# Performance work log

Measured on AMD Instinct MI355X. Metric: run time of the kernel, lower is better.

## Reference

```python
import jax, jax.numpy as jnp
import numpy as np
import math

MODEL_DIM = 512
NUM_HEADS = 8
FFN_DIM = 2048
LN_EPS = 1e-5


def setup_inputs() -> dict:
    key = jax.random.key(0)
    ks = jax.random.split(key, 16)
    B, S, D, F = 1, 4096, MODEL_DIM, FFN_DIM
    s = 1.0 / math.sqrt(D)
    inp = {
        "x": jax.random.normal(ks[0], (B, S, D), dtype=jnp.float32),
        # Linear weights stored [in, out] (transpose of torch's [out, in]); y = x @ W + b
        "wq": jax.random.normal(ks[1], (D, D), dtype=jnp.float32) * s,
        "bq": jnp.zeros((D,), dtype=jnp.float32),
        "wk": jax.random.normal(ks[2], (D, D), dtype=jnp.float32) * s,
        "bk": jnp.zeros((D,), dtype=jnp.float32),
        "wv": jax.random.normal(ks[3], (D, D), dtype=jnp.float32) * s,
        "bv": jnp.zeros((D,), dtype=jnp.float32),
        "wo": jax.random.normal(ks[4], (D, D), dtype=jnp.float32) * s,
        "bo": jnp.zeros((D,), dtype=jnp.float32),
        "w1": jax.random.normal(ks[5], (D, F), dtype=jnp.float32) * s,
        "b1": jnp.zeros((F,), dtype=jnp.float32),
        "w2": jax.random.normal(ks[6], (F, D), dtype=jnp.float32) * (1.0 / math.sqrt(F)),
        "b2": jnp.zeros((D,), dtype=jnp.float32),
        "gamma": jnp.ones((D,), dtype=jnp.float32),
        "beta": jnp.zeros((D,), dtype=jnp.float32),
    }
    return inp


def _layer_norm(x, gamma, beta):
    mu = jnp.mean(x, axis=-1, keepdims=True)
    var = jnp.mean(jnp.square(x - mu), axis=-1, keepdims=True)
    return (x - mu) * jax.lax.rsqrt(var + LN_EPS) * gamma + beta


def reference(x, wq, bq, wk, bk, wv, bv, wo, bo, w1, b1, w2, b2, gamma, beta):
    B, S, D = x.shape
    H = NUM_HEADS
    dph = D // H
    q = x @ wq + bq
    k = x @ wk + bk
    v = x @ wv + bv
    # Faithful to original: direct view [B,S,D] -> [B*H, S, dph] (no head transpose)
    q = q.reshape(B * H, S, dph)
    k = k.reshape(B * H, S, dph)
    v = v.reshape(B * H, S, dph)
    scores = jnp.einsum('bqd,bkd->bqk', q, k) / math.sqrt(dph)  # [B*H, S, S]
    attn = jax.nn.softmax(scores, axis=-1)
    context = jnp.einsum('bqk,bkd->bqd', attn, v).reshape(B, S, D)
    attn_out = context @ wo + bo + x  # residual (dropout is identity in eval)
    ffn = jax.nn.relu(attn_out @ w1 + b1) @ w2 + b2
    out = _layer_norm(ffn + attn_out, gamma, beta)
    return out, attn
```

## Files before the change

### kernel.cpp

```cpp
#include <hip/hip_runtime.h>
#include <hip/hip_bf16.h>
#include <cstdint>
#include <cstddef>

#define SEQ 4096
#define DM  512
#define NH  8
#define DPH 64
#define FF  2048

using short8 = __attribute__((ext_vector_type(8))) short;
using f32x4  = __attribute__((ext_vector_type(4))) float;

__device__ inline float b2f(unsigned short u) {
    union { unsigned int i; float f; } c; c.i = ((unsigned int)u) << 16; return c.f;
}
__device__ inline unsigned short f2b(float f) {
    union { float f; unsigned int u; } c; c.f = f;
    unsigned int u = c.u;
    return (unsigned short)((u + 0x7fffu + ((u >> 16) & 1u)) >> 16);
}

template<int BN, int NI>
__global__ __launch_bounds__(256) void tgemm_kernel(
    const unsigned short* __restrict__ A, const unsigned short* __restrict__ BT,
    const float* __restrict__ bias, const unsigned short* __restrict__ res,
    unsigned short* __restrict__ Cb, float* __restrict__ Cf,
    int M, int N, int K, int relu)
{
    __shared__ __align__(16) unsigned short As[128 * 40];
    __shared__ __align__(16) unsigned short Bs[BN * 40];

    const int t    = threadIdx.x;
    const int lane = t & 63;
    const int wid  = t >> 6;
    const int wr   = wid >> 1, wc = wid & 1;
    const int quad = lane >> 4, cl = lane & 15;
    const int m0 = blockIdx.y * 128;
    const int n0 = blockIdx.x * BN;

    const int srow = t >> 2;
    const int skc  = t & 3;

    const unsigned short* Arow0 = A  + (size_t)(m0 + srow) * K + skc * 8;
    const unsigned short* Arow1 = Arow0 + (size_t)64 * K;
    const unsigned short* Brow0 = BT + (size_t)(n0 + srow) * K + skc * 8;
    const unsigned short* Brow1 = Brow0 + (size_t)64 * K;

    f32x4 acc[4][NI];
    const f32x4 zero4 = {0.f, 0.f, 0.f, 0.f};
#pragma unroll
    for (int mi = 0; mi < 4; ++mi)
#pragma unroll
        for (int ni = 0; ni < NI; ++ni) acc[mi][ni] = zero4;

    short8 ar0, ar1, br0, br1;
    ar0 = *(const short8*)(Arow0);
    ar1 = *(const short8*)(Arow1);
    br0 = *(const short8*)(Brow0);
    if constexpr (NI == 4) br1 = *(const short8*)(Brow1);

    for (int k0 = 0; k0 < K; k0 += 32) {
        __syncthreads();
        *(short8*)(&As[srow * 40 + skc * 8])        = ar0;
        *(short8*)(&As[(srow + 64) * 40 + skc * 8]) = ar1;
        *(short8*)(&Bs[srow * 40 + skc * 8])        = br0;
        if constexpr (NI == 4) *(short8*)(&Bs[(srow + 64) * 40 + skc * 8]) = br1;
        __syncthreads();

        const int kn = k0 + 32;
        if (kn < K) {
            ar0 = *(const short8*)(Arow0 + kn);
            ar1 = *(const short8*)(Arow1 + kn);
            br0 = *(const short8*)(Brow0 + kn);
            if constexpr (NI == 4) br1 = *(const short8*)(Brow1 + kn);
        }

        short8 af[4], bf[NI];
#pragma unroll
        for (int mi = 0; mi < 4; ++mi)
            af[mi] = *(const short8*)(&As[(wr * 64 + mi * 16 + cl) * 40 + quad * 8]);
#pragma unroll
        for (int ni = 0; ni < NI; ++ni)
            bf[ni] = *(const short8*)(&Bs[(wc * (BN / 2) + ni * 16 + cl) * 40 + quad * 8]);
#pragma unroll
        for (int mi = 0; mi < 4; ++mi)
#pragma unroll
            for (int ni = 0; ni < NI; ++ni)
                acc[mi][ni] = __builtin_amdgcn_mfma_f32_16x16x32_bf16(af[mi], bf[ni], acc[mi][ni], 0, 0, 0);
    }

#pragma unroll
    for (int ni = 0; ni < NI; ++ni) {
        const int n = n0 + wc * (BN / 2) + ni * 16 + cl;
        const float bv = bias ? bias[n] : 0.f;
#pragma unroll
        for (int mi = 0; mi < 4; ++mi) {
#pragma unroll
            for (int r = 0; r < 4; ++r) {
                const int row = m0 + wr * 64 + mi * 16 + quad * 4 + r;
                float v = acc[mi][ni][r] + bv;
                const size_t idx = (size_t)row * N + n;
                if (res)  v += b2f(res[idx]);
                if (relu) v = fmaxf(v, 0.f);
                if (Cf) Cf[idx] = v;
                else    Cb[idx] = f2b(v);
            }
        }
    }
}

__global__ __launch_bounds__(256) void transpose_cast_kernel(
    const float* __restrict__ src, unsigned short* __restrict__ dst, int R, int C)
{
    __shared__ float tile[32][33];
    const int c0 = blockIdx.x * 32, r0 = blockIdx.y * 32;
    const int tx = threadIdx.x & 31, ty = threadIdx.x >> 5;
#pragma unroll
    for (int i = 0; i < 4; ++i)
        tile[ty + i * 8][tx] = src[(size_t)(r0 + ty + i * 8) * C + c0 + tx];
    __syncthreads();
#pragma unroll
    for (int i = 0; i < 4; ++i)
        dst[(size_t)(c0 + ty + i * 8) * R + r0 + tx] = f2b(tile[tx][ty + i * 8]);
}

__global__ __launch_bounds__(256) void transpose_kernel(
    const unsigned short* __restrict__ src, unsigned short* __restrict__ dst,
    int R, int C)
{
    __shared__ unsigned short tile[32][33];
    const long off = (long)blockIdx.z * (long)R * (long)C;
    src += off; dst += off;
    const int c0 = blockIdx.x * 32, r0 = blockIdx.y * 32;
    const int tx = threadIdx.x & 31, ty = threadIdx.x >> 5;
#pragma unroll
    for (int i = 0; i < 4; ++i)
        tile[ty + i * 8][tx] = src[(size_t)(r0 + ty + i * 8) * C + c0 + tx];
    __syncthreads();
#pragma unroll
    for (int i = 0; i < 4; ++i)
        dst[(size_t)(c0 + ty + i * 8) * R + r0 + tx] = tile[tx][ty + i * 8];
}

__global__ __launch_bounds__(256) void cast_kernel(
    const float* __restrict__ src, unsigned short* __restrict__ dst, int n4)
{
    const int i = blockIdx.x * 256 + threadIdx.x;
    if (i >= n4) return;
    const float4 v = ((const float4*)src)[i];
    union { unsigned short s[4]; unsigned long long u; } p;
    p.s[0] = f2b(v.x); p.s[1] = f2b(v.y); p.s[2] = f2b(v.z); p.s[3] = f2b(v.w);
    ((unsigned long long*)dst)[i] = p.u;
}

__global__ __launch_bounds__(256, 8) void fused_attn_kernel(
    const unsigned short* __restrict__ qb,
    const unsigned short* __restrict__ kb,
    const unsigned short* __restrict__ vT,
    float* __restrict__ att,
    unsigned short* __restrict__ ctx)
{
    __shared__ __align__(16) float Pl[4][16 * 36];
    __shared__ float smM[4][16];
    __shared__ float smS[4][16];
    __shared__ __align__(16) float cbuf[2][16 * 68];

    const int id    = blockIdx.x;
    const int h     = id & 7;
    const int strip = id >> 3;
    const int lane  = threadIdx.x & 63;
    const int w     = threadIdx.x >> 6;
    const int quad  = lane >> 4, col = lane & 15;
    const int m0    = strip * 16;

    const unsigned short* Qh = qb + (size_t)h * SEQ * DPH;
    const unsigned short* Kh = kb + (size_t)h * SEQ * DPH;
    const unsigned short* Vh = vT + (size_t)h * SEQ * DPH;
    float* atth = att + (size_t)h * SEQ * SEQ;
    unsigned short* ctxh = ctx + (size_t)h * SEQ * DPH;

    const unsigned short* qrow = Qh + (size_t)(m0 + col) * DPH + quad * 8;
    const short8 aq0 = *(const short8*)(qrow);
    const short8 aq1 = *(const short8*)(qrow + 32);

    const unsigned short* kbase = Kh + (size_t)(w * 1024 + col) * DPH + quad * 8;
    const float SC = 0.125f;
    const f32x4 zero4 = {0.f, 0.f, 0.f, 0.f};

    float m[4], s[4];
#pragma unroll
    for (int r = 0; r < 4; ++r) { m[r] = -1e30f; s[r] = 0.f; }

#pragma unroll 2
    for (int nt = 0; nt < 64; ++nt) {
        const unsigned short* kr = kbase + (size_t)nt * 16 * DPH;
        const short8 b0 = *(const short8*)(kr);
        const short8 b1 = *(const short8*)(kr + 32);
        f32x4 acc = zero4;
        acc = __builtin_amdgcn_mfma_f32_16x16x32_bf16(aq0, b0, acc, 0, 0, 0);
        acc = __builtin_amdgcn_mfma_f32_16x16x32_bf16(aq1, b1, acc, 0, 0, 0);
#pragma unroll
        for (int r = 0; r < 4; ++r) {
            const float v  = acc[r] * SC;
            const float nm = fmaxf(m[r], v);
            const float e  = __expf(fminf(m[r], v) - nm);
            s[r] = (v > m[r]) ? fmaf(s[r], e, 1.f) : (s[r] + e);
            m[r] = nm;
        }
    }
#pragma unroll
    for (int off = 1; off < 16; off <<= 1) {
#pragma unroll
        for (int r = 0; r < 4; ++r) {
            const float mo = __shfl_xor(m[r], off);
            const float so = __shfl_xor(s[r], off);
            const float nm = fmaxf(m[r], mo);
            s[r] = s[r] * __expf(m[r] - nm) + so * __expf(mo - nm);
            m[r] = nm;
        }
    }
    if (col == 0) {
#pragma unroll
        for (int r = 0; r < 4; ++r) { smM[w][quad * 4 + r] = m[r]; smS[w][quad * 4 + r] = s[r]; }
    }
    __syncthreads();
    float inv[4];
#pragma unroll
    for (int r = 0; r < 4; ++r) {
        const int row = quad * 4 + r;
        float M = smM[0][row], S = smS[0][row];
#pragma unroll
        for (int ww = 1; ww < 4; ++ww) {
            const float mo = smM[ww][row];
            const float so = smS[ww][row];
            const float nm = fmaxf(M, mo);
            S = S * __expf(M - nm) + so * __expf(mo - nm);
            M = nm;
        }
        m[r] = M;
        inv[r] = 1.f / S;
    }

    f32x4 cacc[4];
#pragma unroll
    for (int t = 0; t < 4; ++t) cacc[t] = zero4;

    float* Pw = Pl[w];
    float* abase = atth + (size_t)m0 * SEQ + w * 1024;
    const int srow2  = lane >> 3;
    const int schunk = lane & 7;
    for (int pr = 0; pr < 32; ++pr) {
#pragma unroll
        for (int sub = 0; sub < 2; ++sub) {
            const int ntl = pr * 2 + sub;
            const unsigned short* kr = kbase + (size_t)ntl * 16 * DPH;
            const short8 b0 = *(const short8*)(kr);
            const short8 b1 = *(const short8*)(kr + 32);
            f32x4 acc = zero4;
            acc = __builtin_amdgcn_mfma_f32_16x16x32_bf16(aq0, b0, acc, 0, 0, 0);
            acc = __builtin_amdgcn_mfma_f32_16x16x32_bf16(aq1, b1, acc, 0, 0, 0);
#pragma unroll
            for (int r = 0; r < 4; ++r) {
                const float p = __expf(fmaf(acc[r], SC, -m[r])) * inv[r];
                Pw[(quad * 4 + r) * 36 + sub * 16 + col] = p;
            }
        }
#pragma unroll
        for (int sset = 0; sset < 2; ++sset) {
            const int prow = srow2 + sset * 8;
            const float4 pv = *(const float4*)(Pw + prow * 36 + schunk * 4);
            *(float4*)(abase + (size_t)prow * SEQ + pr * 32 + schunk * 4) = pv;
        }
        const float4 pa0 = *(const float4*)(Pw + col * 36 + quad * 8);
        const float4 pa1 = *(const float4*)(Pw + col * 36 + quad * 8 + 4);
        union { unsigned short us[8]; short8 v; } ap;
        ap.us[0] = f2b(pa0.x); ap.us[1] = f2b(pa0.y);
        ap.us[2] = f2b(pa0.z); ap.us[3] = f2b(pa0.w);
        ap.us[4] = f2b(pa1.x); ap.us[5] = f2b(pa1.y);
        ap.us[6] = f2b(pa1.z); ap.us[7] = f2b(pa1.w);

        const int kg = w * 1024 + pr * 32;
        const unsigned short* vb0 = Vh + (size_t)col * SEQ + kg + quad * 8;
#pragma unroll
        for (int t = 0; t < 4; ++t) {
            const short8 bv = *(const short8*)(vb0 + (size_t)t * 16 * SEQ);
            cacc[t] = __builtin_amdgcn_mfma_f32_16x16x32_bf16(ap.v, bv, cacc[t], 0, 0, 0);
        }
    }

    if (w & 1) {
        float* cb = cbuf[w >> 1];
#pragma unroll
        for (int t = 0; t < 4; ++t)
#pragma unroll
            for (int r = 0; r < 4; ++r)
                cb[(quad * 4 + r) * 68 + t * 16 + col] = cacc[t][r];
    }
    __syncthreads();
    if (!(w & 1)) {
        const float* cb = cbuf[w >> 1];
#pragma unroll
        for (int t = 0; t < 4; ++t)
#pragma unroll
            for (int r = 0; r < 4; ++r)
                cacc[t][r] += cb[(quad * 4 + r) * 68 + t * 16 + col];
    }
    __syncthreads();
    if (w == 2) {
#pragma unroll
        for (int t = 0; t < 4; ++t)
#pragma unroll
            for (int r = 0; r < 4; ++r)
                cbuf[0][(quad * 4 + r) * 68 + t * 16 + col] = cacc[t][r];
    }
    __syncthreads();
    if (w == 0) {
#pragma unroll
        for (int t = 0; t < 4; ++t) {
#pragma unroll
            for (int r = 0; r < 4; ++r) {
                const float v = cacc[t][r] + cbuf[0][(quad * 4 + r) * 68 + t * 16 + col];
                ctxh[(size_t)(m0 + quad * 4 + r) * DPH + t * 16 + col] = f2b(v);
            }
        }
    }
}

__global__ __launch_bounds__(256) void ln_kernel(
    const float* __restrict__ pre,
    const float* __restrict__ gamma, const float* __restrict__ beta,
    float* __restrict__ out)
{
    __shared__ float redS[4], redQ[4];
    const float* p = pre + (size_t)blockIdx.x * 512;
    const int t = threadIdx.x;
    const int w = t >> 6, lane = t & 63;

    const float2 xv = *(const float2*)(p + t * 2);
    float s = xv.x + xv.y;
    float q = xv.x * xv.x + xv.y * xv.y;
#pragma unroll
    for (int off = 32; off; off >>= 1) {
        s += __shfl_xor(s, off);
        q += __shfl_xor(q, off);
    }
    if (lane == 0) { redS[w] = s; redQ[w] = q; }
    __syncthreads();
    s = redS[0] + redS[1] + redS[2] + redS[3];
    q = redQ[0] + redQ[1] + redQ[2] + redQ[3];

    const float mu  = s * (1.f / 512.f);
    const float var = q * (1.f / 512.f) - mu * mu;
    const float rs  = rsqrtf(var + 1e-5f);

    const size_t o = (size_t)blockIdx.x * 512 + t * 2;
    out[o]     = (xv.x - mu) * rs * gamma[t * 2]     + beta[t * 2];
    out[o + 1] = (xv.y - mu) * rs * gamma[t * 2 + 1] + beta[t * 2 + 1];
}

extern "C" void kernel_launch(void* const* d_in, const int* in_sizes, int n_in,
                              void* d_out, int out_size, void* d_ws, size_t ws_size,
                              hipStream_t stream)
{
    (void)in_sizes; (void)n_in; (void)out_size; (void)ws_size;

    const float* x     = (const float*)d_in[0];
    const float* wq    = (const float*)d_in[1];
    const float* bq    = (const float*)d_in[2];
    const float* wk    = (const float*)d_in[3];
    const float* bk    = (const float*)d_in[4];
    const float* wv    = (const float*)d_in[5];
    const float* bv    = (const float*)d_in[6];
    const float* wo    = (const float*)d_in[7];
    const float* bo    = (const float*)d_in[8];
    const float* w1    = (const float*)d_in[9];
    const float* b1    = (const float*)d_in[10];
    const float* w2    = (const float*)d_in[11];
    const float* b2    = (const float*)d_in[12];
    const float* gamma = (const float*)d_in[13];
    const float* beta  = (const float*)d_in[14];

    float* out = (float*)d_out;
    float* att = out + (size_t)SEQ * DM;

    char* wsp = (char*)d_ws;
    auto alloc = [&](size_t bytes) {
        char* p = wsp;
        wsp += (bytes + 255) & ~(size_t)255;
        return p;
    };
    unsigned short* wqT  = (unsigned short*)alloc((size_t)DM * DM * 2);
    unsigned short* wkT  = (unsigned short*)alloc((size_t)DM * DM * 2);
    unsigned short* wvT  = (unsigned short*)alloc((size_t)DM * DM * 2);
    unsigned short* woT  = (unsigned short*)alloc((size_t)DM * DM * 2);
    unsigned short* w1T  = (unsigned short*)alloc((size_t)DM * FF * 2);
    unsigned short* w2T  = (unsigned short*)alloc((size_t)FF * DM * 2);
    unsigned short* xb   = (unsigned short*)alloc((size_t)SEQ * DM * 2);
    unsigned short* qb   = (unsigned short*)alloc((size_t)SEQ * DM * 2);
    unsigned short* kb   = (unsigned short*)alloc((size_t)SEQ * DM * 2);
    unsigned short* vb   = (unsigned short*)alloc((size_t)SEQ * DM * 2);
    unsigned short* vT   = (unsigned short*)alloc((size_t)SEQ * DM * 2);
    unsigned short* ctx  = (unsigned short*)alloc((size_t)SEQ * DM * 2);
    unsigned short* aout = (unsigned short*)alloc((size_t)SEQ * DM * 2);
    unsigned short* ffn1 = (unsigned short*)alloc((size_t)SEQ * FF * 2);
    float*          pre  = (float*)alloc((size_t)SEQ * DM * 4);

    const dim3 blk(256);

    cast_kernel<<<dim3((SEQ * DM / 4 + 255) / 256), blk, 0, stream>>>(x, xb, SEQ * DM / 4);

    transpose_cast_kernel<<<dim3(16, 16), blk, 0, stream>>>(wq, wqT, DM, DM);
    transpose_cast_kernel<<<dim3(16, 16), blk, 0, stream>>>(wk, wkT, DM, DM);
    transpose_cast_kernel<<<dim3(16, 16), blk, 0, stream>>>(wv, wvT, DM, DM);
    transpose_cast_kernel<<<dim3(16, 16), blk, 0, stream>>>(wo, woT, DM, DM);
    transpose_cast_kernel<<<dim3(64, 16), blk, 0, stream>>>(w1, w1T, DM, FF);
    transpose_cast_kernel<<<dim3(16, 64), blk, 0, stream>>>(w2, w2T, FF, DM);

    tgemm_kernel<64, 2><<<dim3(8, 32), blk, 0, stream>>>(xb, wqT, bq, nullptr, qb, nullptr,
                                                         SEQ, DM, DM, 0);
    tgemm_kernel<64, 2><<<dim3(8, 32), blk, 0, stream>>>(xb, wkT, bk, nullptr, kb, nullptr,
                                                         SEQ, DM, DM, 0);
    tgemm_kernel<64, 2><<<dim3(8, 32), blk, 0, stream>>>(xb, wvT, bv, nullptr, vb, nullptr,
                                                         SEQ, DM, DM, 0);

    transpose_kernel<<<dim3(2, 128, 8), blk, 0, stream>>>(vb, vT, SEQ, DPH);

    fused_attn_kernel<<<dim3(2048), blk, 0, stream>>>(qb, kb, vT, att, ctx);

    tgemm_kernel<64, 2><<<dim3(8, 32), blk, 0, stream>>>(ctx, woT, bo, xb, aout, nullptr,
                                                         SEQ, DM, DM, 0);

    tgemm_kernel<128, 4><<<dim3(16, 32), blk, 0, stream>>>(aout, w1T, b1, nullptr, ffn1, nullptr,
                                                           SEQ, FF, DM, 1);

    tgemm_kernel<64, 2><<<dim3(8, 32), blk, 0, stream>>>(ffn1, w2T, b2, aout, nullptr, pre,
                                                         SEQ, DM, FF, 0);

    ln_kernel<<<dim3(SEQ), blk, 0, stream>>>(pre, gamma, beta, out);
}
```

Before: 982.5 us.

## Fuse QKV GEMM, split attention-prob writeback into separate kernel, shrink GEMM tiles

Concatenates the Q/K/V weights and biases so one GEMM launch produces all three projections, with the epilogue routing each column section to its own buffer. The fused attention kernel no longer writes the full SxS probability matrix. It saves per-row max and inverse sum, and a new att_write_kernel recomputes QK^T and streams the normalized probabilities out with wide stores. The GEMM template is generalised to BM/BN tiles, and the 512-wide GEMMs now use 64x64 tiles for more blocks. The cost is recomputing the score matmul in exchange for decoupling the large attention-matrix write from the softmax-V pipeline.

Result: slower. 1.073 ms (+9.2%).

```diff
diff --git a/kernel.cpp b/kernel.cpp
--- a/kernel.cpp
+++ b/kernel.cpp
@@ -21,14 +21,19 @@
     return (unsigned short)((u + 0x7fffu + ((u >> 16) & 1u)) >> 16);
 }
 
-template<int BN, int NI>
+template<int BM, int BN, int QKV>
 __global__ __launch_bounds__(256) void tgemm_kernel(
     const unsigned short* __restrict__ A, const unsigned short* __restrict__ BT,
     const float* __restrict__ bias, const unsigned short* __restrict__ res,
     unsigned short* __restrict__ Cb, float* __restrict__ Cf,
+    unsigned short* __restrict__ Ck, unsigned short* __restrict__ Cv,
     int M, int N, int K, int relu)
 {
-    __shared__ __align__(16) unsigned short As[128 * 40];
+    constexpr int MI  = BM / 32;
+    constexpr int NI  = BN / 32;
+    constexpr int CPT = (BM + BN) / 64;
+
+    __shared__ __align__(16) unsigned short As[BM * 40];
     __shared__ __align__(16) unsigned short Bs[BN * 40];
 
     const int t    = threadIdx.x;
@@ -36,55 +41,56 @@
     const int wid  = t >> 6;
     const int wr   = wid >> 1, wc = wid & 1;
     const int quad = lane >> 4, cl = lane & 15;
-    const int m0 = blockIdx.y * 128;
+    const int m0 = blockIdx.y * BM;
     const int n0 = blockIdx.x * BN;
 
-    const int srow = t >> 2;
-    const int skc  = t & 3;
-
-    const unsigned short* Arow0 = A  + (size_t)(m0 + srow) * K + skc * 8;
-    const unsigned short* Arow1 = Arow0 + (size_t)64 * K;
-    const unsigned short* Brow0 = BT + (size_t)(n0 + srow) * K + skc * 8;
-    const unsigned short* Brow1 = Brow0 + (size_t)64 * K;
-
-    f32x4 acc[4][NI];
+    const unsigned short* gsrc[CPT];
+    unsigned short*       ldst[CPT];
+#pragma unroll
+    for (int i = 0; i < CPT; ++i) {
+        const int c = t + i * 256;
+        const int row = c >> 2, kc = c & 3;
+        if (row < BM) {
+            gsrc[i] = A + (size_t)(m0 + row) * K + kc * 8;
+            ldst[i] = As + row * 40 + kc * 8;
+        } else {
+            gsrc[i] = BT + (size_t)(n0 + row - BM) * K + kc * 8;
+            ldst[i] = Bs + (row - BM) * 40 + kc * 8;
+        }
+    }
+
+    f32x4 acc[MI][NI];
     const f32x4 zero4 = {0.f, 0.f, 0.f, 0.f};
 #pragma unroll
-    for (int mi = 0; mi < 4; ++mi)
+    for (int mi = 0; mi < MI; ++mi)
 #pragma unroll
         for (int ni = 0; ni < NI; ++ni) acc[mi][ni] = zero4;
 
-    short8 ar0, ar1, br0, br1;
-    ar0 = *(const short8*)(Arow0);
-    ar1 = *(const short8*)(Arow1);
-    br0 = *(const short8*)(Brow0);
-    if constexpr (NI == 4) br1 = *(const short8*)(Brow1);
+    short8 pf[CPT];
+#pragma unroll
+    for (int i = 0; i < CPT; ++i) pf[i] = *(const short8*)(gsrc[i]);
 
     for (int k0 = 0; k0 < K; k0 += 32) {
         __syncthreads();
-        *(short8*)(&As[srow * 40 + skc * 8])        = ar0;
-        *(short8*)(&As[(srow + 64) * 40 + skc * 8]) = ar1;
-        *(short8*)(&Bs[srow * 40 + skc * 8])        = br0;
-        if constexpr (NI == 4) *(short8*)(&Bs[(srow + 64) * 40 + skc * 8]) = br1;
+#pragma unroll
+        for (int i = 0; i < CPT; ++i) *(short8*)(ldst[i]) = pf[i];
         __syncthreads();
 
         const int kn = k0 + 32;
         if (kn < K) {
-            ar0 = *(const short8*)(Arow0 + kn);
-            ar1 = *(const short8*)(Arow1 + kn);
-            br0 = *(const short8*)(Brow0 + kn);
-            if constexpr (NI == 4) br1 = *(const short8*)(Brow1 + kn);
-        }
-
-        short8 af[4], bf[NI];
-#pragma unroll
-        for (int mi = 0; mi < 4; ++mi)
-            af[mi] = *(const short8*)(&As[(wr * 64 + mi * 16 + cl) * 40 + quad * 8]);
+#pragma unroll
+            for (int i = 0; i < CPT; ++i) pf[i] = *(const short8*)(gsrc[i] + kn);
+        }
+
+        short8 af[MI], bf[NI];
+#pragma unroll
+        for (int mi = 0; mi < MI; ++mi)
+            af[mi] = *(const short8*)(&As[(wr * (BM / 2) + mi * 16 + cl) * 40 + quad * 8]);
 #pragma unroll
         for (int ni = 0; ni < NI; ++ni)
             bf[ni] = *(const short8*)(&Bs[(wc * (BN / 2) + ni * 16 + cl) * 40 + quad * 8]);
 #pragma unroll
-        for (int mi = 0; mi < 4; ++mi)
+        for (int mi = 0; mi < MI; ++mi)
 #pragma unroll
             for (int ni = 0; ni < NI; ++ni)
                 acc[mi][ni] = __builtin_amdgcn_mfma_f32_16x16x32_bf16(af[mi], bf[ni], acc[mi][ni], 0, 0, 0);
@@ -95,16 +101,22 @@
         const int n = n0 + wc * (BN / 2) + ni * 16 + cl;
         const float bv = bias ? bias[n] : 0.f;
 #pragma unroll
-        for (int mi = 0; mi < 4; ++mi) {
+        for (int mi = 0; mi < MI; ++mi) {
 #pragma unroll
             for (int r = 0; r < 4; ++r) {
-                const int row = m0 + wr * 64 + mi * 16 + quad * 4 + r;
+                const int row = m0 + wr * (BM / 2) + mi * 16 + quad * 4 + r;
                 float v = acc[mi][ni][r] + bv;
-                const size_t idx = (size_t)row * N + n;
-                if (res)  v += b2f(res[idx]);
-                if (relu) v = fmaxf(v, 0.f);
-                if (Cf) Cf[idx] = v;
-                else    Cb[idx] = f2b(v);
+                if (QKV) {
+                    const int sec = n >> 9, nc = n & 511;
+                    unsigned short* dst = sec == 0 ? Cb : (sec == 1 ? Ck : Cv);
+                    dst[(size_t)row * 512 + nc] = f2b(v);
+                } else {
+                    const size_t idx = (size_t)row * N + n;
+                    if (res)  v += b2f(res[idx]);
+                    if (relu) v = fmaxf(v, 0.f);
+                    if (Cf) Cf[idx] = v;
+                    else    Cb[idx] = f2b(v);
+                }
             }
         }
     }
@@ -154,12 +166,22 @@
     ((unsigned long long*)dst)[i] = p.u;
 }
 
+__global__ __launch_bounds__(256) void bias_concat_kernel(
+    const float* __restrict__ bq, const float* __restrict__ bk,
+    const float* __restrict__ bv, float* __restrict__ bqkv)
+{
+    const int i = blockIdx.x * 256 + threadIdx.x;
+    if (i >= 1536) return;
+    bqkv[i] = i < 512 ? bq[i] : (i < 1024 ? bk[i - 512] : bv[i - 1024]);
+}
+
 __global__ __launch_bounds__(256, 8) void fused_attn_kernel(
     const unsigned short* __restrict__ qb,
     const unsigned short* __restrict__ kb,
     const unsigned short* __restrict__ vT,
-    float* __restrict__ att,
-    unsigned short* __restrict__ ctx)
+    unsigned short* __restrict__ ctx,
+    float* __restrict__ m_ws,
+    float* __restrict__ inv_ws)
 {
     __shared__ __align__(16) float Pl[4][16 * 36];
     __shared__ float smM[4][16];
@@ -177,7 +199,6 @@
     const unsigned short* Qh = qb + (size_t)h * SEQ * DPH;
     const unsigned short* Kh = kb + (size_t)h * SEQ * DPH;
     const unsigned short* Vh = vT + (size_t)h * SEQ * DPH;
-    float* atth = att + (size_t)h * SEQ * SEQ;
     unsigned short* ctxh = ctx + (size_t)h * SEQ * DPH;
 
     const unsigned short* qrow = Qh + (size_t)(m0 + col) * DPH + quad * 8;
@@ -241,15 +262,19 @@
         m[r] = M;
         inv[r] = 1.f / S;
     }
+    if (w == 0 && col == 0) {
+#pragma unroll
+        for (int r = 0; r < 4; ++r) {
+            m_ws[(size_t)h * SEQ + m0 + quad * 4 + r]   = m[r];
+            inv_ws[(size_t)h * SEQ + m0 + quad * 4 + r] = inv[r];
+        }
+    }
 
     f32x4 cacc[4];
 #pragma unroll
     for (int t = 0; t < 4; ++t) cacc[t] = zero4;
 
     float* Pw = Pl[w];
-    float* abase = atth + (size_t)m0 * SEQ + w * 1024;
-    const int srow2  = lane >> 3;
-    const int schunk = lane & 7;
     for (int pr = 0; pr < 32; ++pr) {
 #pragma unroll
         for (int sub = 0; sub < 2; ++sub) {
@@ -266,12 +291,6 @@
                 Pw[(quad * 4 + r) * 36 + sub * 16 + col] = p;
             }
         }
-#pragma unroll
-        for (int sset = 0; sset < 2; ++sset) {
-            const int prow = srow2 + sset * 8;
-            const float4 pv = *(const float4*)(Pw + prow * 36 + schunk * 4);
-            *(float4*)(abase + (size_t)prow * SEQ + pr * 32 + schunk * 4) = pv;
-        }
         const float4 pa0 = *(const float4*)(Pw + col * 36 + quad * 8);
         const float4 pa1 = *(const float4*)(Pw + col * 36 + quad * 8 + 4);
         union { unsigned short us[8]; short8 v; } ap;
@@ -323,6 +342,80 @@
                 const float v = cacc[t][r] + cbuf[0][(quad * 4 + r) * 68 + t * 16 + col];
                 ctxh[(size_t)(m0 + quad * 4 + r) * DPH + t * 16 + col] = f2b(v);
             }
+        }
+    }
+}
+
+__global__ __launch_bounds__(256) void att_write_kernel(
+    const unsigned short* __restrict__ qb,
+    const unsigned short* __restrict__ kb,
+    const float* __restrict__ m_ws, const float* __restrict__ inv_ws,
+    float* __restrict__ att)
+{
+    __shared__ __align__(16) float Pl[4][16 * 36];
+
+    const int id   = blockIdx.x;
+    const int h    = id & 7;
+    const int rt   = id >> 3;
+    const int ct   = rt & 15;
+    const int rb   = rt >> 4;
+    const int lane = threadIdx.x & 63;
+    const int w    = threadIdx.x >> 6;
+    const int quad = lane >> 4, col = lane & 15;
+    const int m0   = rb * 64 + w * 16;
+    const int c0   = ct * 256;
+
+    const unsigned short* Qh = qb + (size_t)h * SEQ * DPH;
+    const unsigned short* Kh = kb + (size_t)h * SEQ * DPH;
+    float* atth = att + (size_t)h * SEQ * SEQ;
+
+    const unsigned short* qrow = Qh + (size_t)(m0 + col) * DPH + quad * 8;
+    const short8 aq0 = *(const short8*)(qrow);
+    const short8 aq1 = *(const short8*)(qrow + 32);
+
+    float mrow[4], invr[4];
+#pragma unroll
+    for (int r = 0; r < 4; ++r) {
+        mrow[r] = m_ws[(size_t)h * SEQ + m0 + quad * 4 + r];
+        invr[r] = inv_ws[(size_t)h * SEQ + m0 + quad * 4 + r];
+    }
+
+    const unsigned short* kbase = Kh + (size_t)(c0 + col) * DPH + quad * 8;
+    const float SC = 0.125f;
+    const f32x4 zero4 = {0.f, 0.f, 0.f, 0.f};
+
+    f32x4 p[16];
+#pragma unroll
+    for (int t = 0; t < 16; ++t) {
+        const unsigned short* kr = kbase + (size_t)t * 16 * DPH;
+        const short8 b0 = *(const short8*)(kr);
+        const short8 b1 = *(const short8*)(kr + 32);
+        f32x4 acc = zero4;
+        acc = __builtin_amdgcn_mfma_f32_16x16x32_bf16(aq0, b0, acc, 0, 0, 0);
+        acc = __builtin_amdgcn_mfma_f32_16x16x32_bf16(aq1, b1, acc, 0, 0, 0);
+#pragma unroll
+        for (int r = 0; r < 4; ++r)
+            p[t][r] = __expf(fmaf(acc[r], SC, -mrow[r])) * invr[r];
+    }
+
+    float* Pw = Pl[w];
+    const int srow2  = lane >> 3;
+    const int schunk = lane & 7;
+    float* abase = atth + (size_t)m0 * SEQ + c0;
+#pragma unroll
+    for (int g = 0; g < 8; ++g) {
+#pragma unroll
+        for (int half = 0; half < 2; ++half) {
+            const int t = g * 2 + half;
+#pragma unroll
+            for (int r = 0; r < 4; ++r)
+                Pw[(quad * 4 + r) * 36 + half * 16 + col] = p[t][r];
+        }
+#pragma unroll
+        for (int sset = 0; sset < 2; ++sset) {
+            const int prow = srow2 + sset * 8;
+            const float4 pv = *(const float4*)(Pw + prow * 36 + schunk * 4);
+            *(float4*)(abase + (size_t)prow * SEQ + g * 32 + schunk * 4) = pv;
         }
     }
 }
@@ -390,52 +483,52 @@
         wsp += (bytes + 255) & ~(size_t)255;
         return p;
     };
-    unsigned short* wqT  = (unsigned short*)alloc((size_t)DM * DM * 2);
-    unsigned short* wkT  = (unsigned short*)alloc((size_t)DM * DM * 2);
-    unsigned short* wvT  = (unsigned short*)alloc((size_t)DM * DM * 2);
-    unsigned short* woT  = (unsigned short*)alloc((size_t)DM * DM * 2);
-    unsigned short* w1T  = (unsigned short*)alloc((size_t)DM * FF * 2);
-    unsigned short* w2T  = (unsigned short*)alloc((size_t)FF * DM * 2);
-    unsigned short* xb   = (unsigned short*)alloc((size_t)SEQ * DM * 2);
-    unsigned short* qb   = (unsigned short*)alloc((size_t)SEQ * DM * 2);
-    unsigned short* kb   = (unsigned short*)alloc((size_t)SEQ * DM * 2);
-    unsigned short* vb   = (unsigned short*)alloc((size_t)SEQ * DM * 2);
-    unsigned short* vT   = (unsigned short*)alloc((size_t)SEQ * DM * 2);
-    unsigned short* ctx  = (unsigned short*)alloc((size_t)SEQ * DM * 2);
-    unsigned short* aout = (unsigned short*)alloc((size_t)SEQ * DM * 2);
-    unsigned short* ffn1 = (unsigned short*)alloc((size_t)SEQ * FF * 2);
-    float*          pre  = (float*)alloc((size_t)SEQ * DM * 4);
+    unsigned short* wqkvT = (unsigned short*)alloc((size_t)3 * DM * DM * 2);
+    unsigned short* woT   = (unsigned short*)alloc((size_t)DM * DM * 2);
+    unsigned short* w1T   = (unsigned short*)alloc((size_t)DM * FF * 2);
+    unsigned short* w2T   = (unsigned short*)alloc((size_t)FF * DM * 2);
+    unsigned short* xb    = (unsigned short*)alloc((size_t)SEQ * DM * 2);
+    unsigned short* qb    = (unsigned short*)alloc((size_t)SEQ * DM * 2);
+    unsigned short* kb    = (unsigned short*)alloc((size_t)SEQ * DM * 2);
+    unsigned short* vb    = (unsigned short*)alloc((size_t)SEQ * DM * 2);
+    unsigned short* vT    = (unsigned short*)alloc((size_t)SEQ * DM * 2);
+    unsigned short* ctx   = (unsigned short*)alloc((size_t)SEQ * DM * 2);
+    unsigned short* aout  = (unsigned short*)alloc((size_t)SEQ * DM * 2);
+    unsigned short* ffn1  = (unsigned short*)alloc((size_t)SEQ * FF * 2);
+    float*          pre   = (float*)alloc((size_t)SEQ * DM * 4);
+    float*          bqkv  = (float*)alloc((size_t)3 * DM * 4);
+    float*          m_ws  = (float*)alloc((size_t)NH * SEQ * 4);
+    float*          i_ws  = (float*)alloc((size_t)NH * SEQ * 4);
 
     const dim3 blk(256);
 
     cast_kernel<<<dim3((SEQ * DM / 4 + 255) / 256), blk, 0, stream>>>(x, xb, SEQ * DM / 4);
 
-    transpose_cast_kernel<<<dim3(16, 16), blk, 0, stream>>>(wq, wqT, DM, DM);
-    transpose_cast_kernel<<<dim3(16, 16), blk, 0, stream>>>(wk, wkT, DM, DM);
-    transpose_cast_kernel<<<dim3(16, 16), blk, 0, stream>>>(wv, wvT, DM, DM);
+    transpose_cast_kernel<<<dim3(16, 16), blk, 0, stream>>>(wq, wqkvT, DM, DM);
+    transpose_cast_kernel<<<dim3(16, 16), blk, 0, stream>>>(wk, wqkvT + (size_t)DM * DM, DM, DM);
+    transpose_cast_kernel<<<dim3(16, 16), blk, 0, stream>>>(wv, wqkvT + (size_t)2 * DM * DM, DM, DM);
     transpose_cast_kernel<<<dim3(16, 16), blk, 0, stream>>>(wo, woT, DM, DM);
     transpose_cast_kernel<<<dim3(64, 16), blk, 0, stream>>>(w1, w1T, DM, FF);
     transpose_cast_kernel<<<dim3(16, 64), blk, 0, stream>>>(w2, w2T, FF, DM);
-
-    tgemm_kernel<64, 2><<<dim3(8, 32), blk, 0, stream>>>(xb, wqT, bq, nullptr, qb, nullptr,
-                                                         SEQ, DM, DM, 0);
-    tgemm_kernel<64, 2><<<dim3(8, 32), blk, 0, stream>>>(xb, wkT, bk, nullptr, kb, nullptr,
-                                                         SEQ, DM, DM, 0);
-    tgemm_kernel<64, 2><<<dim3(8, 32), blk, 0, stream>>>(xb, wvT, bv, nullptr, vb, nullptr,
-                                                         SEQ, DM, DM, 0);
+    bias_concat_kernel<<<dim3(6), blk, 0, stream>>>(bq, bk, bv, bqkv);
+
+    tgemm_kernel<64, 64, 1><<<dim3(24, 64), blk, 0, stream>>>(
+        xb, wqkvT, bqkv, nullptr, qb, nullptr, kb, vb, SEQ, 3 * DM, DM, 0);
 
     transpose_kernel<<<dim3(2, 128, 8), blk, 0, stream>>>(vb, vT, SEQ, DPH);
 
-    fused_attn_kernel<<<dim3(2048), blk, 0, stream>>>(qb, kb, vT, att, ctx);
-
-    tgemm_kernel<64, 2><<<dim3(8, 32), blk, 0, stream>>>(ctx, woT, bo, xb, aout, nullptr,
-                                                         SEQ, DM, DM, 0);
-
-    tgemm_kernel<128, 4><<<dim3(16, 32), blk, 0, stream>>>(aout, w1T, b1, nullptr, ffn1, nullptr,
-                                                           SEQ, FF, DM, 1);
-
-    tgemm_kernel<64, 2><<<dim3(8, 32), blk, 0, stream>>>(ffn1, w2T, b2, aout, nullptr, pre,
-                                                         SEQ, DM, FF, 0);
+    fused_attn_kernel<<<dim3(2048), blk, 0, stream>>>(qb, kb, vT, ctx, m_ws, i_ws);
+
+    att_write_kernel<<<dim3(8192), blk, 0, stream>>>(qb, kb, m_ws, i_ws, att);
+
+    tgemm_kernel<64, 64, 0><<<dim3(8, 64), blk, 0, stream>>>(
+        ctx, woT, bo, xb, aout, nullptr, nullptr, nullptr, SEQ, DM, DM, 0);
+
+    tgemm_kernel<128, 128, 0><<<dim3(16, 32), blk, 0, stream>>>(
+        aout, w1T, b1, nullptr, ffn1, nullptr, nullptr, nullptr, SEQ, FF, DM, 1);
+
+    tgemm_kernel<64, 64, 0><<<dim3(8, 64), blk, 0, stream>>>(
+        ffn1, w2T, b2, aout, nullptr, pre, nullptr, nullptr, SEQ, DM, FF, 0);
 
     ln_kernel<<<dim3(SEQ), blk, 0, stream>>>(pre, gamma, beta, out);
 }
```
